# Performance work log

Hardware: AMD Instinct MI355X
Metric: run time of the kernel (lower is better)

## Reference

```python
import jax, jax.numpy as jnp
import numpy as np

HIDDEN = 64
N_HEADS = 4
TOP_K = 10
ALPHA = 0.3


def setup_inputs() -> dict:
    key = jax.random.key(0)
    ks = jax.random.split(key, 12)
    B, N, T, Dd, Ds, H = 4, 2048, 32, 16, 8, HIDDEN
    s = lambda i, shape, scale: (jax.random.normal(ks[i], shape, dtype=jnp.float32) * scale)
    return {
        "x_dyn": jax.random.normal(ks[0], (B, N, T, Dd), dtype=jnp.float32),
        "x_stat": jax.random.normal(ks[1], (B, N, Ds), dtype=jnp.float32),
        "A_prior": jax.random.uniform(ks[2], (B, N, N), dtype=jnp.float32),
        "W_dyn": s(3, (Dd, H), 1.0 / np.sqrt(Dd)),
        "b_dyn": jnp.zeros((H,), jnp.float32),
        "W_stat": s(4, (Ds, H), 1.0 / np.sqrt(Ds)),
        "b_stat": jnp.zeros((H,), jnp.float32),
        "W_fuse": s(5, (2 * H, H), 1.0 / np.sqrt(2 * H)),
        "b_fuse": jnp.zeros((H,), jnp.float32),
        "Wq": s(6, (H, H), 1.0 / np.sqrt(H)),
        "Wk": s(7, (H, H), 1.0 / np.sqrt(H)),
    }


def reference(x_dyn, x_stat, A_prior, W_dyn, b_dyn, W_stat, b_stat, W_fuse, b_fuse, Wq, Wk):
    B, N = x_dyn.shape[0], x_dyn.shape[1]
    H, nh = HIDDEN, N_HEADS
    dh = H // nh

    # TemporalEncoder: linear + mean over time + ReLU -> (B, N, H)
    h = jax.nn.relu(jnp.mean(x_dyn @ W_dyn + b_dyn, axis=2))
    # FeatureEncoder: linear + ReLU -> (B, N, H)
    h_s = jax.nn.relu(x_stat @ W_stat + b_stat)
    # Fusion
    h = jnp.concatenate([h, h_s], axis=-1) @ W_fuse + b_fuse

    # GraphAttention: multi-head softmax(QK^T / sqrt(dh)) averaged over heads
    q = (h @ Wq).reshape(B, N, nh, dh)
    k = (h @ Wk).reshape(B, N, nh, dh)
    scores = jnp.einsum("bnhd,bmhd->bhnm", q, k) / jnp.sqrt(jnp.float32(dh))
    A_learn = jnp.mean(jax.nn.softmax(scores, axis=-1), axis=1)  # (B, N, N)

    # Top-k mask along last dim (scatter 1s at topk indices)
    _, topk_inds = jax.lax.top_k(A_learn, TOP_K)  # (B, N, k)
    b_idx = jnp.arange(B)[:, None, None]
    n_idx = jnp.arange(N)[None, :, None]
    mask = jnp.zeros_like(A_learn).at[b_idx, n_idx, topk_inds].set(1.0)
    A_sparse = A_learn * mask
    A_learn = (A_sparse + jnp.swapaxes(A_sparse, 1, 2)) * 0.5

    # Blend with prior
    A_final = ALPHA * A_prior + (1.0 - ALPHA) * A_learn

    # Laplacian L = D - A
    degree = jnp.sum(A_final, axis=-1)  # (B, N)
    eye = jnp.eye(N, dtype=A_final.dtype)
    L = degree[..., None] * eye - A_final
    return (L, A_final)
```

## Files before the change

kernel.cpp:

```cpp
#include <hip/hip_runtime.h>

#define NBATCH 4
#define NN 2048
#define NR 8192
#define TOPK 10
#define CSTRIDE 161

typedef __attribute__((ext_vector_type(16))) float f32x16;
typedef __attribute__((ext_vector_type(8))) short bf16x8;

__device__ inline unsigned short f2bf(float x) {
    unsigned u = __float_as_uint(x);
    unsigned r = (u + 0x7FFF + ((u >> 16) & 1)) >> 16;
    return (unsigned short)r;
}

__global__ __launch_bounds__(256) void k1_encode(
    const float* __restrict__ xd, const float* __restrict__ xs,
    const float* __restrict__ Wd, const float* __restrict__ bd,
    const float* __restrict__ Ws, const float* __restrict__ bs,
    const float* __restrict__ Wf, const float* __restrict__ bf,
    const float* __restrict__ Wq, const float* __restrict__ Wk,
    unsigned short* __restrict__ qh, unsigned short* __restrict__ kh)
{
    int wave = threadIdx.x >> 6;
    int lane = threadIdx.x & 63;
    int r = blockIdx.x * 4 + wave;

    __shared__ float xm[4][16];
    __shared__ float xst[4][8];
    __shared__ float hc[4][128];
    __shared__ float hh[4][64];

    const float* xdr = xd + (size_t)r * 512;
    float acc = 0.f;
    #pragma unroll
    for (int j = 0; j < 8; ++j) acc += xdr[lane + 64*j];
    acc += __shfl_xor(acc, 16);
    acc += __shfl_xor(acc, 32);
    if (lane < 16) xm[wave][lane] = acc * (1.0f/32.0f);
    if (lane < 8)  xst[wave][lane] = xs[(size_t)r*8 + lane];
    __syncthreads();

    float a1 = bd[lane];
    #pragma unroll
    for (int d = 0; d < 16; ++d) a1 += xm[wave][d] * Wd[d*64 + lane];
    a1 = fmaxf(a1, 0.f);
    float a2 = bs[lane];
    #pragma unroll
    for (int d = 0; d < 8; ++d) a2 += xst[wave][d] * Ws[d*64 + lane];
    a2 = fmaxf(a2, 0.f);
    hc[wave][lane] = a1;
    hc[wave][64 + lane] = a2;
    __syncthreads();

    float hv0 = bf[lane], hv1 = 0.f, hv2 = 0.f, hv3 = 0.f;
    #pragma unroll
    for (int j = 0; j < 128; j += 4) {
        hv0 += hc[wave][j]   * Wf[(j)*64   + lane];
        hv1 += hc[wave][j+1] * Wf[(j+1)*64 + lane];
        hv2 += hc[wave][j+2] * Wf[(j+2)*64 + lane];
        hv3 += hc[wave][j+3] * Wf[(j+3)*64 + lane];
    }
    hh[wave][lane] = (hv0 + hv1) + (hv2 + hv3);
    __syncthreads();

    float qv0 = 0.f, qv1 = 0.f, kv0 = 0.f, kv1 = 0.f;
    #pragma unroll
    for (int j = 0; j < 64; j += 2) {
        float h0 = hh[wave][j], h1 = hh[wave][j+1];
        qv0 += h0 * Wq[(j)*64   + lane];
        qv1 += h1 * Wq[(j+1)*64 + lane];
        kv0 += h0 * Wk[(j)*64   + lane];
        kv1 += h1 * Wk[(j+1)*64 + lane];
    }
    float qv = qv0 + qv1, kv = kv0 + kv1;
    int b = r >> 11, n = r & 2047;
    int head = lane >> 4, dim = lane & 15;
    size_t base = ((size_t)(b*4 + head) * NN + n) * 16;
    qh[base + dim] = f2bf(qv);
    kh[base + dim] = f2bf(kv);
}

__global__ __launch_bounds__(512, 4) void k23(
    const unsigned short* __restrict__ qh, const unsigned short* __restrict__ kh,
    unsigned* __restrict__ winners, float* __restrict__ diagw,
    const float* __restrict__ prior, float* __restrict__ Lout,
    float* __restrict__ Aout)
{
    const float C1 = 0.36067376022224085f;
    int tid = threadIdx.x;

    if (blockIdx.x >= 256) {
        int r = blockIdx.x - 256;
        __shared__ float wsum[8];
        const float4* pr = (const float4*)(prior + (size_t)r * NN);
        float4* Ar = (float4*)(Aout + (size_t)r * NN);
        float4* Lr = (float4*)(Lout + (size_t)r * NN);
        float4 p = pr[tid];
        float4 a; a.x = 0.3f*p.x; a.y = 0.3f*p.y; a.z = 0.3f*p.z; a.w = 0.3f*p.w;
        Ar[tid] = a;
        float4 lv; lv.x = -a.x; lv.y = -a.y; lv.z = -a.z; lv.w = -a.w;
        Lr[tid] = lv;
        float sum = a.x + a.y + a.z + a.w;
        #pragma unroll
        for (int o = 32; o > 0; o >>= 1) sum += __shfl_down(sum, o);
        if ((tid & 63) == 0) wsum[tid >> 6] = sum;
        __syncthreads();
        if (tid == 0) {
            float tot = 0.f;
            #pragma unroll
            for (int ww = 0; ww < 8; ++ww) tot += wsum[ww];
            atomicAdd(&Lout[(size_t)r * NN + (r & 2047)], tot);
        }
        return;
    }

    int b  = blockIdx.x >> 6;
    int rg = blockIdx.x & 63;
    int w = tid >> 6, l = tid & 63;
    int row = l & 31, khalf = l >> 5;

    __shared__ unsigned cand[32 * CSTRIDE];
    __shared__ float redS[8][4][32];
    __shared__ float r4s[4][32];

    bf16x8 qfrag[4];
    #pragma unroll
    for (int h = 0; h < 4; ++h)
        qfrag[h] = *(const bf16x8*)(qh + ((size_t)(b*4+h) * NN + rg*32 + row) * 16 + khalf*8);

    float Sl[4] = {0.f, 0.f, 0.f, 0.f};
    for (int t = 0; t < 8; ++t) {
        int m0 = w*256 + t*32;
        #pragma unroll
        for (int h = 0; h < 4; ++h) {
            bf16x8 kfrag = *(const bf16x8*)(kh + ((size_t)(b*4+h) * NN + m0 + row) * 16 + khalf*8);
            f32x16 acc = {0.f,0.f,0.f,0.f,0.f,0.f,0.f,0.f,0.f,0.f,0.f,0.f,0.f,0.f,0.f,0.f};
            acc = __builtin_amdgcn_mfma_f32_32x32x16_bf16(kfrag, qfrag[h], acc, 0, 0, 0);
            #pragma unroll
            for (int rr = 0; rr < 16; ++rr) Sl[h] += exp2f(acc[rr] * C1);
        }
    }
    #pragma unroll
    for (int h = 0; h < 4; ++h) Sl[h] += __shfl_xor(Sl[h], 32);
    if (l < 32) {
        #pragma unroll
        for (int h = 0; h < 4; ++h) redS[w][h][l] = Sl[h];
    }
    __syncthreads();
    if (tid < 128) {
        int h = tid >> 5, rw = tid & 31;
        float s = 0.f;
        #pragma unroll
        for (int ww = 0; ww < 8; ++ww) s += redS[ww][h][rw];
        r4s[h][rw] = 0.25f / s;
    }
    __syncthreads();

    float r4[4];
    #pragma unroll
    for (int h = 0; h < 4; ++h) r4[h] = r4s[h][row];

    unsigned tkl[TOPK];
    #pragma unroll
    for (int s = 0; s < TOPK; ++s) tkl[s] = 0u;
    for (int t = 0; t < 8; ++t) {
        int m0 = w*256 + t*32;
        float vacc[16];
        #pragma unroll
        for (int rr = 0; rr < 16; ++rr) vacc[rr] = 0.f;
        #pragma unroll
        for (int h = 0; h < 4; ++h) {
            bf16x8 kfrag = *(const bf16x8*)(kh + ((size_t)(b*4+h) * NN + m0 + row) * 16 + khalf*8);
            f32x16 acc = {0.f,0.f,0.f,0.f,0.f,0.f,0.f,0.f,0.f,0.f,0.f,0.f,0.f,0.f,0.f,0.f};
            acc = __builtin_amdgcn_mfma_f32_32x32x16_bf16(kfrag, qfrag[h], acc, 0, 0, 0);
            #pragma unroll
            for (int rr = 0; rr < 16; ++rr)
                vacc[rr] = fmaf(exp2f(acc[rr] * C1), r4[h], vacc[rr]);
        }
        #pragma unroll
        for (int rr = 0; rr < 16; ++rr) {
            int c = m0 + ((rr & 3) + 8*(rr >> 2) + 4*khalf);
            unsigned key = ((unsigned)f2bf(vacc[rr]) << 16) | (unsigned)(2047 - c);
            if (key > tkl[TOPK-1]) {
                unsigned ck = key;
                #pragma unroll
                for (int s = 0; s < TOPK; ++s) {
                    bool ins = ck > tkl[s];
                    unsigned o = tkl[s];
                    tkl[s] = ins ? ck : o;
                    ck     = ins ? o  : ck;
                }
            }
        }
    }
    {
        unsigned* cr = &cand[row * CSTRIDE + (w*2 + khalf) * TOPK];
        #pragma unroll
        for (int s = 0; s < TOPK; ++s) cr[s] = tkl[s];
    }
    __syncthreads();

    #pragma unroll 1
    for (int rr2 = 0; rr2 < 4; ++rr2) {
        int prow = w*4 + rr2;
        const unsigned* flat = &cand[prow * CSTRIDE];
        unsigned t0 = flat[l];
        unsigned t1 = flat[l + 64];
        unsigned t2 = (l < 32) ? flat[l + 128] : 0u;
        if (t1 > t0) { unsigned x = t0; t0 = t1; t1 = x; }
        if (t2 > t1) { unsigned x = t1; t1 = t2; t2 = x; }
        if (t1 > t0) { unsigned x = t0; t0 = t1; t1 = x; }
        unsigned mykey = 0u;
        #pragma unroll 1
        for (int s = 0; s < TOPK; ++s) {
            unsigned kmax = t0;
            #pragma unroll
            for (int d = 1; d < 64; d <<= 1) {
                unsigned o = __shfl_xor(kmax, d);
                kmax = (o > kmax) ? o : kmax;
            }
            if (t0 == kmax) { t0 = t1; t1 = t2; t2 = 0u; }
            if (l == s) mykey = kmax;
        }

        int n = rg*32 + prow;
        int r = b*NN + n;
        float wv = (l < TOPK) ? 0.35f * __uint_as_float(mykey & 0xFFFF0000u) : 0.f;
        float swv = wv;
        #pragma unroll
        for (int d = 1; d <= 8; d <<= 1) swv += __shfl_xor(swv, d);
        if (l == 0) diagw[r] = swv;
        if (l < TOPK) winners[(size_t)l * NR + r] = mykey;
    }
}

__global__ __launch_bounds__(256) void k4_scatter(
    const unsigned* __restrict__ winners, const float* __restrict__ diagw,
    float* __restrict__ Lout, float* __restrict__ Aout)
{
    int wk = blockIdx.x * 256 + threadIdx.x;
    int s = wk >> 13;
    int r = wk & 8191;
    int b = r >> 11;
    int n = r & 2047;
    unsigned key = winners[(size_t)s * NR + r];
    float wv = 0.35f * __uint_as_float(key & 0xFFFF0000u);
    int j = 2047 - (int)(key & 0x7FFu);
    size_t rbase = (size_t)r * NN;
    size_t jbase = (size_t)(b * NN + j) * NN;
    atomicAdd(&Aout[rbase + j],  wv);
    atomicAdd(&Aout[jbase + n],  wv);
    atomicAdd(&Lout[rbase + j], -wv);
    atomicAdd(&Lout[jbase + n], -wv);
    atomicAdd(&Lout[jbase + j],  wv);
    if (s == 0) atomicAdd(&Lout[rbase + n], diagw[r]);
}

extern "C" void kernel_launch(void* const* d_in, const int* in_sizes, int n_in,
                              void* d_out, int out_size, void* d_ws, size_t ws_size,
                              hipStream_t stream)
{
    const float* xd    = (const float*)d_in[0];
    const float* xs    = (const float*)d_in[1];
    const float* prior = (const float*)d_in[2];
    const float* Wd    = (const float*)d_in[3];
    const float* bd    = (const float*)d_in[4];
    const float* Ws    = (const float*)d_in[5];
    const float* bs    = (const float*)d_in[6];
    const float* Wf    = (const float*)d_in[7];
    const float* bf    = (const float*)d_in[8];
    const float* Wq    = (const float*)d_in[9];
    const float* Wk    = (const float*)d_in[10];

    float* Lout = (float*)d_out;
    float* Aout = Lout + (size_t)NR * NN;

    unsigned short* qh = (unsigned short*)d_ws;
    unsigned short* kh = qh + (size_t)16 * NN * 16;
    unsigned* winners  = (unsigned*)(kh + (size_t)16 * NN * 16);
    float* diagw       = (float*)(winners + (size_t)TOPK * NR);

    k1_encode<<<NR/4, 256, 0, stream>>>(xd, xs, Wd, bd, Ws, bs, Wf, bf, Wq, Wk, qh, kh);
    k23<<<256 + NR, 512, 0, stream>>>(qh, kh, winners, diagw, prior, Lout, Aout);
    k4_scatter<<<TOPK*NR/256, 256, 0, stream>>>(winners, diagw, Lout, Aout);
}
```

Before: 303.6 us.

## Double k23 block size to 16 waves per row group and pack prior rows

The attention/top-k kernel now launches 1024-thread blocks, so 16 waves each scan 128 columns instead of 8 waves scanning 256. This halves the serial MFMA/exp/top-k work per wave but doubles the candidates merged per row. The merge now has each lane hold 5 sorted candidates from a 320-entry list. The prior-blend blocks each handle two rows, halving their block count. The shorter per-wave loop comes at the cost of more shared memory, larger reductions, and lower occupancy limits with 1024-thread blocks.

```diff
diff --git a/kernel.cpp b/kernel.cpp
--- a/kernel.cpp
+++ b/kernel.cpp
@@ -4,7 +4,7 @@
 #define NN 2048
 #define NR 8192
 #define TOPK 10
-#define CSTRIDE 161
+#define CSTRIDE 321
 
 typedef __attribute__((ext_vector_type(16))) float f32x16;
 typedef __attribute__((ext_vector_type(8))) short bf16x8;
@@ -82,7 +82,7 @@
     kh[base + dim] = f2bf(kv);
 }
 
-__global__ __launch_bounds__(512, 4) void k23(
+__global__ __launch_bounds__(1024, 4) void k23(
     const unsigned short* __restrict__ qh, const unsigned short* __restrict__ kh,
     unsigned* __restrict__ winners, float* __restrict__ diagw,
     const float* __restrict__ prior, float* __restrict__ Lout,
@@ -92,25 +92,26 @@
     int tid = threadIdx.x;
 
     if (blockIdx.x >= 256) {
-        int r = blockIdx.x - 256;
-        __shared__ float wsum[8];
+        int g = tid >> 9, t = tid & 511;
+        int r = (blockIdx.x - 256) * 2 + g;
+        __shared__ float wsum[16];
         const float4* pr = (const float4*)(prior + (size_t)r * NN);
         float4* Ar = (float4*)(Aout + (size_t)r * NN);
         float4* Lr = (float4*)(Lout + (size_t)r * NN);
-        float4 p = pr[tid];
+        float4 p = pr[t];
         float4 a; a.x = 0.3f*p.x; a.y = 0.3f*p.y; a.z = 0.3f*p.z; a.w = 0.3f*p.w;
-        Ar[tid] = a;
+        Ar[t] = a;
         float4 lv; lv.x = -a.x; lv.y = -a.y; lv.z = -a.z; lv.w = -a.w;
-        Lr[tid] = lv;
+        Lr[t] = lv;
         float sum = a.x + a.y + a.z + a.w;
         #pragma unroll
         for (int o = 32; o > 0; o >>= 1) sum += __shfl_down(sum, o);
         if ((tid & 63) == 0) wsum[tid >> 6] = sum;
         __syncthreads();
-        if (tid == 0) {
+        if (t == 0) {
             float tot = 0.f;
             #pragma unroll
-            for (int ww = 0; ww < 8; ++ww) tot += wsum[ww];
+            for (int ww = 0; ww < 8; ++ww) tot += wsum[g*8 + ww];
             atomicAdd(&Lout[(size_t)r * NN + (r & 2047)], tot);
         }
         return;
@@ -122,7 +123,7 @@
     int row = l & 31, khalf = l >> 5;
 
     __shared__ unsigned cand[32 * CSTRIDE];
-    __shared__ float redS[8][4][32];
+    __shared__ float redS[16][4][32];
     __shared__ float r4s[4][32];
 
     bf16x8 qfrag[4];
@@ -131,8 +132,8 @@
         qfrag[h] = *(const bf16x8*)(qh + ((size_t)(b*4+h) * NN + rg*32 + row) * 16 + khalf*8);
 
     float Sl[4] = {0.f, 0.f, 0.f, 0.f};
-    for (int t = 0; t < 8; ++t) {
-        int m0 = w*256 + t*32;
+    for (int t = 0; t < 4; ++t) {
+        int m0 = w*128 + t*32;
         #pragma unroll
         for (int h = 0; h < 4; ++h) {
             bf16x8 kfrag = *(const bf16x8*)(kh + ((size_t)(b*4+h) * NN + m0 + row) * 16 + khalf*8);
@@ -153,7 +154,7 @@
         int h = tid >> 5, rw = tid & 31;
         float s = 0.f;
         #pragma unroll
-        for (int ww = 0; ww < 8; ++ww) s += redS[ww][h][rw];
+        for (int ww = 0; ww < 16; ++ww) s += redS[ww][h][rw];
         r4s[h][rw] = 0.25f / s;
     }
     __syncthreads();
@@ -165,8 +166,8 @@
     unsigned tkl[TOPK];
     #pragma unroll
     for (int s = 0; s < TOPK; ++s) tkl[s] = 0u;
-    for (int t = 0; t < 8; ++t) {
-        int m0 = w*256 + t*32;
+    for (int t = 0; t < 4; ++t) {
+        int m0 = w*128 + t*32;
         float vacc[16];
         #pragma unroll
         for (int rr = 0; rr < 16; ++rr) vacc[rr] = 0.f;
@@ -203,25 +204,26 @@
     __syncthreads();
 
     #pragma unroll 1
-    for (int rr2 = 0; rr2 < 4; ++rr2) {
-        int prow = w*4 + rr2;
+    for (int rr2 = 0; rr2 < 2; ++rr2) {
+        int prow = w*2 + rr2;
         const unsigned* flat = &cand[prow * CSTRIDE];
-        unsigned t0 = flat[l];
-        unsigned t1 = flat[l + 64];
-        unsigned t2 = (l < 32) ? flat[l + 128] : 0u;
-        if (t1 > t0) { unsigned x = t0; t0 = t1; t1 = x; }
-        if (t2 > t1) { unsigned x = t1; t1 = t2; t2 = x; }
-        if (t1 > t0) { unsigned x = t0; t0 = t1; t1 = x; }
+        unsigned tk5[5];
+        #pragma unroll
+        for (int i = 0; i < 5; ++i) tk5[i] = flat[l*5 + i];
         unsigned mykey = 0u;
         #pragma unroll 1
         for (int s = 0; s < TOPK; ++s) {
-            unsigned kmax = t0;
+            unsigned kmax = tk5[0];
             #pragma unroll
             for (int d = 1; d < 64; d <<= 1) {
                 unsigned o = __shfl_xor(kmax, d);
                 kmax = (o > kmax) ? o : kmax;
             }
-            if (t0 == kmax) { t0 = t1; t1 = t2; t2 = 0u; }
+            if (tk5[0] == kmax) {
+                #pragma unroll
+                for (int q = 0; q < 4; ++q) tk5[q] = tk5[q+1];
+                tk5[4] = 0u;
+            }
             if (l == s) mykey = kmax;
         }
 
@@ -283,6 +285,6 @@
     float* diagw       = (float*)(winners + (size_t)TOPK * NR);
 
     k1_encode<<<NR/4, 256, 0, stream>>>(xd, xs, Wd, bd, Ws, bs, Wf, bf, Wq, Wk, qh, kh);
-    k23<<<256 + NR, 512, 0, stream>>>(qh, kh, winners, diagw, prior, Lout, Aout);
+    k23<<<256 + NR/2, 1024, 0, stream>>>(qh, kh, winners, diagw, prior, Lout, Aout);
     k4_scatter<<<TOPK*NR/256, 256, 0, stream>>>(winners, diagw, Lout, Aout);
 }
```

Measured after the change: 331.5 us. 1.09x slower.
